# Kernel tuning notes

Measured on AMD Instinct MI355X. Metric: run time of the kernel, lower is better.

The kernel has to match this reference:

```python
import jax, jax.numpy as jnp
import numpy as np

IN_F, OUT_F, R = 4096, 4096, 16
SCALING = 32.0 / R  # lora_alpha / r


def setup_inputs() -> dict:
    key = jax.random.key(0)
    kx, kw, kb, ka, kB = jax.random.split(key, 5)
    bound_w = 1.0 / np.sqrt(IN_F)  # kaiming_uniform a=sqrt(5) on (out,in) -> U(-1/sqrt(in), 1/sqrt(in))
    x = jax.random.normal(kx, (4, 4096, IN_F), dtype=jnp.float32)
    weight = jax.random.uniform(kw, (OUT_F, IN_F), jnp.float32, -bound_w, bound_w)
    bias = jax.random.uniform(kb, (OUT_F,), jnp.float32, -bound_w, bound_w)
    lora_A = jax.random.uniform(ka, (R, IN_F), jnp.float32, -bound_w, bound_w)
    # B is zero-init in the module; use small random values so the LoRA path is exercised
    lora_B = jax.random.normal(kB, (OUT_F, R), dtype=jnp.float32) * 0.01
    return {"x": x, "weight": weight, "bias": bias, "lora_A": lora_A, "lora_B": lora_B}


def reference(x, weight, bias, lora_A, lora_B):
    # base: F.linear(x, W, b) = x @ W.T + b
    base_out = jnp.einsum("bsi,oi->bso", x, weight) + bias
    # low-rank path: (x @ A.T) @ B.T * scaling  (dropout=0 -> identity)
    xr = jnp.einsum("bsi,ri->bsr", x, lora_A)  # [b, s, r]
    lora_out = jnp.einsum("bsr,or->bso", xr, lora_B) * SCALING
    return base_out + lora_out
```

## Files before the change

### kernel.cpp

```cpp
#include <hip/hip_runtime.h>
#include <hip/hip_bf16.h>


typedef __attribute__((ext_vector_type(8))) short bf16x8;
typedef __attribute__((ext_vector_type(4))) float f32x4;
typedef __attribute__((ext_vector_type(4))) unsigned short u16x4;

#define M_DIM 16384
#define N_DIM 4096
#define K_DIM 4096
#define NT 64

__device__ __forceinline__ unsigned short f2bf(float f) {
    unsigned int u = __builtin_bit_cast(unsigned int, f);
    unsigned int r = u + 0x7FFFu + ((u >> 16) & 1u);
    return (unsigned short)(r >> 16);
}

__device__ __forceinline__ void async16(const void* g, void* l) {
    __builtin_amdgcn_global_load_lds(
        (const __attribute__((address_space(1))) unsigned int*)g,
        (__attribute__((address_space(3))) unsigned int*)l,
        16, 0, 0);
}

__global__ void __launch_bounds__(256) cast_x_kernel(
    const float4* __restrict__ x, u16x4* __restrict__ y, int n4) {
    int i = blockIdx.x * blockDim.x + threadIdx.x;
    int stride = gridDim.x * blockDim.x;
    for (; i < n4; i += stride) {
        float4 v = x[i];
        u16x4 o = { f2bf(v.x), f2bf(v.y), f2bf(v.z), f2bf(v.w) };
        y[i] = o;
    }
}

__global__ void __launch_bounds__(256) weff_kernel(
    const float* __restrict__ W, const float* __restrict__ lA,
    const float* __restrict__ lB, unsigned short* __restrict__ out) {
    constexpr int K = K_DIM, R = 16;
    constexpr float S = 2.0f;
    int o = blockIdx.x;
    int t = threadIdx.x;
    float b[R];
#pragma unroll
    for (int r = 0; r < R; ++r) b[r] = lB[o * R + r];
#pragma unroll
    for (int c = 0; c < 4; ++c) {
        int i = c * 1024 + t * 4;
        float4 wv = *reinterpret_cast<const float4*>(&W[o * K + i]);
        float sx = 0.f, sy = 0.f, sz = 0.f, sw = 0.f;
#pragma unroll
        for (int r = 0; r < R; ++r) {
            float4 a = *reinterpret_cast<const float4*>(&lA[r * K + i]);
            sx += b[r] * a.x; sy += b[r] * a.y;
            sz += b[r] * a.z; sw += b[r] * a.w;
        }
        u16x4 ov = { f2bf(wv.x + S * sx), f2bf(wv.y + S * sy),
                     f2bf(wv.z + S * sz), f2bf(wv.w + S * sw) };
        *reinterpret_cast<u16x4*>(&out[o * K + i]) = ov;
    }
}

#define STAGE(G, h, tt, bsel, moff)                                           \
    do {                                                                      \
        const unsigned short* g0 = (G) +                                      \
            (size_t)((h) * 128 + wid * 16 + rc) * K_DIM + (tt) * 64 + cc * 8; \
        char* l0 = lds + (bsel) * 65536 + (moff) + (h) * 16384 + wid * 2048;  \
        async16(g0, l0);                                                      \
        async16(g0 + 8 * K_DIM, l0 + 1024);                                   \
    } while (0)

#define LDA_KS(dst, mh, ks, bsel)                                             \
    _Pragma("unroll") for (int mm = 0; mm < 4; ++mm)                          \
        dst[mm] = *(const bf16x8*)(lds + (bsel) * 65536 +                     \
            ((aBase + ((mh) * 4 + mm) * 2048) ^ ((ks) << 6)));

#define LDB_KS(ks, bsel)                                                      \
    _Pragma("unroll") for (int nn = 0; nn < 4; ++nn)                          \
        br[nn][ks] = *(const bf16x8*)(lds + (bsel) * 65536 +                  \
            ((bBase + nn * 2048) ^ ((ks) << 6)));

#define MMQ_KS(src, mh, ks)                                                   \
    __builtin_amdgcn_s_setprio(1);                                            \
    _Pragma("unroll") for (int mm = 0; mm < 4; ++mm)                          \
    _Pragma("unroll") for (int nn = 0; nn < 4; ++nn)                          \
        acc[(mh) * 4 + mm][nn] = __builtin_amdgcn_mfma_f32_16x16x32_bf16(     \
            src[mm], br[nn][ks], acc[(mh) * 4 + mm][nn], 0, 0, 0);            \
    __builtin_amdgcn_s_setprio(0)

#define CFENCE() asm volatile("" ::: "memory")
#define WAIT_LGKM(n)                                                          \
    asm volatile("s_waitcnt lgkmcnt(" #n ")" ::: "memory");                   \
    __builtin_amdgcn_sched_barrier(0)

#define KTILE(t)                                                              \
    {                                                                         \
        const int bs_ = (t) & 1, bo_ = bs_ ^ 1;                               \
        LDA_KS(arE, 0, 0, bs_);                                   \
        LDB_KS(0, bs_);                                           \
        if ((t) + 1 < NT) STAGE(Ag, 0, (t) + 1, bo_, 0);                      \
        LDA_KS(arO, 1, 0, bs_);                                    \
        WAIT_LGKM(4);                                                         \
        MMQ_KS(arE, 0, 0);                                                    \
        if ((t) + 1 < NT) STAGE(Ag, 1, (t) + 1, bo_, 0);                      \
        LDA_KS(arE, 0, 1, bs_);                \
        LDB_KS(1, bs_);                                           \
        WAIT_LGKM(8);                                                         \
        MMQ_KS(arO, 1, 0);                                                    \
        LDA_KS(arO, 1, 1, bs_);                                    \
        WAIT_LGKM(4);                                                         \
        MMQ_KS(arE, 0, 1);                                                    \
        CFENCE();                                                             \
        __builtin_amdgcn_s_barrier();    \
        CFENCE();                                                             \
        if ((t) + 2 < NT) STAGE(Bg, 0, (t) + 2, bs_, 32768);                  \
        WAIT_LGKM(0);                                                         \
        MMQ_KS(arO, 1, 1);                                                    \
        if ((t) + 2 < NT) STAGE(Bg, 1, (t) + 2, bs_, 32768);                  \
        if ((t) < NT - 2) {                                                   \
            asm volatile("s_waitcnt vmcnt(4)" ::: "memory");                  \
        } else {                                                              \
            asm volatile("s_waitcnt vmcnt(0)" ::: "memory");                  \
        }                                                                     \
        __builtin_amdgcn_s_barrier();                                         \
        CFENCE();                                                             \
    }

__global__ void __launch_bounds__(512, 2) gemmks_kernel(
    const unsigned short* __restrict__ A,
    const unsigned short* __restrict__ B,
    const float* __restrict__ bias,
    float* __restrict__ C) {
    __shared__ __align__(1024) char lds[131072];

    const int tid = threadIdx.x;
    const int lane = tid & 63, wid = tid >> 6;
    const int wm = wid >> 2, wn = wid & 3;
    const int lr = lane & 15, lg = lane >> 4;

    const int bid = blockIdx.x;
    const int swz = (bid & 7) * 128 + (bid >> 3);
    const int bm = swz >> 4, bn = swz & 15;

    const unsigned short* Ag = A + (size_t)bm * 256 * K_DIM;
    const unsigned short* Bg = B + (size_t)bn * 256 * K_DIM;

    const int lam = lane ^ (lane >> 3);
    const int rc = lam >> 3, cc = lam & 7;

    const int kx0 = (lg * 16) ^ ((lr & 7) << 4);
    const int aBase = (wm * 128 + lr) * 128 + kx0;
    const int bBase = 32768 + (wn * 64 + lr) * 128 + kx0;

    f32x4 acc[8][4] = {};
    bf16x8 arE[4], arO[4], br[4][2];

    STAGE(Bg, 0, 0, 0, 32768);
    STAGE(Bg, 1, 0, 0, 32768);
    STAGE(Ag, 0, 0, 0, 0);
    STAGE(Ag, 1, 0, 0, 0);
    STAGE(Bg, 0, 1, 1, 32768);
    STAGE(Bg, 1, 1, 1, 32768);
    asm volatile("s_waitcnt vmcnt(4)" ::: "memory");
    __builtin_amdgcn_s_barrier();
    CFENCE();

#pragma unroll 2
    for (int t = 0; t < NT; ++t) {
        KTILE(t);
    }

    const int row0 = bm * 256 + wm * 128;
    const int col0 = bn * 256 + wn * 64;
#pragma unroll
    for (int n = 0; n < 4; ++n) {
        const int col = col0 + n * 16 + lr;
        const float bv = bias[col];
#pragma unroll
        for (int m = 0; m < 8; ++m) {
            const int r0 = row0 + m * 16 + lg * 4;
#pragma unroll
            for (int r = 0; r < 4; ++r)
                C[(size_t)(r0 + r) * N_DIM + col] = acc[m][n][r] + bv;
        }
    }
}

extern "C" void kernel_launch(void* const* d_in, const int* in_sizes, int n_in,
                              void* d_out, int out_size, void* d_ws, size_t ws_size,
                              hipStream_t stream) {
    const float* x    = (const float*)d_in[0];
    const float* W    = (const float*)d_in[1];
    const float* bias = (const float*)d_in[2];
    const float* lA   = (const float*)d_in[3];
    const float* lB   = (const float*)d_in[4];
    float* out = (float*)d_out;

    unsigned short* xb   = (unsigned short*)d_ws;
    unsigned short* weff = (unsigned short*)((char*)d_ws + 134217728);

    cast_x_kernel<<<2048, 256, 0, stream>>>((const float4*)x, (u16x4*)xb,
                                            M_DIM * K_DIM / 4);
    weff_kernel<<<N_DIM, 256, 0, stream>>>(W, lA, lB, weff);
    gemmks_kernel<<<(M_DIM / 256) * (N_DIM / 256), 512, 0, stream>>>(
        xb, weff, bias, out);
}
```

Measured before the change: 593.2 us.

## Pre-swizzle operands into MFMA fragment layout and switch to 32x32x16 MFMA

The cast and weight-fusion kernels now write bf16 operands directly in a fragment-major layout, so each 32x16 MFMA fragment is a contiguous 1 KB block. The GEMM can then stage with simple linear async copies and read LDS without XOR swizzles. It also moves from 16x16x32 to 32x32x16 MFMA instructions, which need fewer instructions and fewer LDS reads per unit of work. In exchange, the cast kernel's global reads become less coalesced, accumulators now take 16-float vectors, and the epilogue store pattern changes.

```diff
diff --git a/kernel.cpp b/kernel.cpp
--- a/kernel.cpp
+++ b/kernel.cpp
@@ -3,7 +3,7 @@
 
 
 typedef __attribute__((ext_vector_type(8))) short bf16x8;
-typedef __attribute__((ext_vector_type(4))) float f32x4;
+typedef __attribute__((ext_vector_type(16))) float f32x16;
 typedef __attribute__((ext_vector_type(4))) unsigned short u16x4;
 
 #define M_DIM 16384
@@ -25,13 +25,20 @@
 }
 
 __global__ void __launch_bounds__(256) cast_x_kernel(
-    const float4* __restrict__ x, u16x4* __restrict__ y, int n4) {
-    int i = blockIdx.x * blockDim.x + threadIdx.x;
-    int stride = gridDim.x * blockDim.x;
-    for (; i < n4; i += stride) {
-        float4 v = x[i];
-        u16x4 o = { f2bf(v.x), f2bf(v.y), f2bf(v.z), f2bf(v.w) };
-        y[i] = o;
+    const float* __restrict__ x, unsigned short* __restrict__ y) {
+    const int total = 512 * 256 * 64;
+    int idx = blockIdx.x * 256 + threadIdx.x;
+    const int stride = gridDim.x * 256;
+    for (; idx < total; idx += stride) {
+        const int frag = idx >> 6, l = idx & 63;
+        const int m = ((frag >> 8) << 5) + (l & 31);
+        const int k = ((frag & 255) << 4) + ((l >> 5) << 3);
+        const float4* px = reinterpret_cast<const float4*>(&x[(size_t)m * K_DIM + k]);
+        float4 a = px[0], b = px[1];
+        unsigned short r[8] = { f2bf(a.x), f2bf(a.y), f2bf(a.z), f2bf(a.w),
+                                f2bf(b.x), f2bf(b.y), f2bf(b.z), f2bf(b.w) };
+        *reinterpret_cast<bf16x8*>(&y[((size_t)frag << 9) + (l << 3)]) =
+            *reinterpret_cast<const bf16x8*>(r);
     }
 }
 
@@ -58,35 +65,50 @@
         }
         u16x4 ov = { f2bf(wv.x + S * sx), f2bf(wv.y + S * sy),
                      f2bf(wv.z + S * sz), f2bf(wv.w + S * sw) };
-        *reinterpret_cast<u16x4*>(&out[o * K + i]) = ov;
-    }
-}
-
-#define STAGE(G, h, tt, bsel, moff)                                           \
-    do {                                                                      \
-        const unsigned short* g0 = (G) +                                      \
-            (size_t)((h) * 128 + wid * 16 + rc) * K_DIM + (tt) * 64 + cc * 8; \
-        char* l0 = lds + (bsel) * 65536 + (moff) + (h) * 16384 + wid * 2048;  \
-        async16(g0, l0);                                                      \
-        async16(g0 + 8 * K_DIM, l0 + 1024);                                   \
-    } while (0)
-
-#define LDA_KS(dst, mh, ks, bsel)                                             \
-    _Pragma("unroll") for (int mm = 0; mm < 4; ++mm)                          \
-        dst[mm] = *(const bf16x8*)(lds + (bsel) * 65536 +                     \
-            ((aBase + ((mh) * 4 + mm) * 2048) ^ ((ks) << 6)));
-
-#define LDB_KS(ks, bsel)                                                      \
-    _Pragma("unroll") for (int nn = 0; nn < 4; ++nn)                          \
-        br[nn][ks] = *(const bf16x8*)(lds + (bsel) * 65536 +                  \
-            ((bBase + nn * 2048) ^ ((ks) << 6)));
-
-#define MMQ_KS(src, mh, ks)                                                   \
+        const int frag = (o >> 5) * 256 + (i >> 4);
+        const int lane_ = (o & 31) + (((i >> 3) & 1) << 5);
+        *reinterpret_cast<u16x4*>(
+            &out[((size_t)frag << 9) + (lane_ << 3) + (i & 7)]) = ov;
+    }
+}
+
+#define ASTAGE(t, bsel, jlo, jhi)                                             \
+    _Pragma("unroll") for (int j = (jlo); j <= (jhi); ++j) {                  \
+        const int g = wid * 4 + j;                                            \
+        async16(A + (((size_t)(bm * 8 + (g >> 2)) * 256 + (t) * 4 + (g & 3))  \
+                     << 9) + (lane << 3),                                     \
+                lds + (bsel) * 65536 + g * 1024 + (lane << 4));               \
+    }
+
+#define BSTAGE(t, bsel)                                                       \
+    _Pragma("unroll") for (int j = 0; j < 4; ++j) {                           \
+        const int g = wid * 4 + j;                                            \
+        async16(B + (((size_t)(bn * 8 + (g >> 2)) * 256 + (t) * 4 + (g & 3))  \
+                     << 9) + (lane << 3),                                     \
+                lds + (bsel) * 65536 + 32768 + g * 1024 + (lane << 4));       \
+    }
+
+#define LDA32(dst, mh, kh, bsel)                                              \
+    _Pragma("unroll") for (int mm = 0; mm < 2; ++mm)                          \
+    _Pragma("unroll") for (int kk = 0; kk < 2; ++kk)                          \
+        dst[mm * 2 + kk] = *(const bf16x8*)(lds + (bsel) * 65536 +            \
+            (((wm * 4 + (mh) * 2 + mm) * 4 + (kh) * 2 + kk) << 10) +          \
+            (lane << 4));
+
+#define LDB32(dst, kh, bsel)                                                  \
+    _Pragma("unroll") for (int nn = 0; nn < 2; ++nn)                          \
+    _Pragma("unroll") for (int kk = 0; kk < 2; ++kk)                          \
+        dst[nn * 2 + kk] = *(const bf16x8*)(lds + (bsel) * 65536 + 32768 +    \
+            (((wn * 2 + nn) * 4 + (kh) * 2 + kk) << 10) + (lane << 4));
+
+#define MMQ(asrc, bsrc, mh)                                                   \
     __builtin_amdgcn_s_setprio(1);                                            \
-    _Pragma("unroll") for (int mm = 0; mm < 4; ++mm)                          \
-    _Pragma("unroll") for (int nn = 0; nn < 4; ++nn)                          \
-        acc[(mh) * 4 + mm][nn] = __builtin_amdgcn_mfma_f32_16x16x32_bf16(     \
-            src[mm], br[nn][ks], acc[(mh) * 4 + mm][nn], 0, 0, 0);            \
+    _Pragma("unroll") for (int kk = 0; kk < 2; ++kk)                          \
+    _Pragma("unroll") for (int mm = 0; mm < 2; ++mm)                          \
+    _Pragma("unroll") for (int nn = 0; nn < 2; ++nn)                          \
+        acc[(mh) * 2 + mm][nn] = __builtin_amdgcn_mfma_f32_32x32x16_bf16(     \
+            asrc[mm * 2 + kk], bsrc[nn * 2 + kk], acc[(mh) * 2 + mm][nn],     \
+            0, 0, 0);                                                         \
     __builtin_amdgcn_s_setprio(0)
 
 #define CFENCE() asm volatile("" ::: "memory")
@@ -97,27 +119,26 @@
 #define KTILE(t)                                                              \
     {                                                                         \
         const int bs_ = (t) & 1, bo_ = bs_ ^ 1;                               \
-        LDA_KS(arE, 0, 0, bs_);                                   \
-        LDB_KS(0, bs_);                                           \
-        if ((t) + 1 < NT) STAGE(Ag, 0, (t) + 1, bo_, 0);                      \
-        LDA_KS(arO, 1, 0, bs_);                                    \
+        LDA32(arE, 0, 0, bs_);                                    \
+        LDB32(br0, 0, bs_);                                       \
+        if ((t) + 1 < NT) ASTAGE((t) + 1, bo_, 0, 1);                         \
+        LDA32(arO, 1, 0, bs_);                                     \
         WAIT_LGKM(4);                                                         \
-        MMQ_KS(arE, 0, 0);                                                    \
-        if ((t) + 1 < NT) STAGE(Ag, 1, (t) + 1, bo_, 0);                      \
-        LDA_KS(arE, 0, 1, bs_);                \
-        LDB_KS(1, bs_);                                           \
+        MMQ(arE, br0, 0);                                                     \
+        if ((t) + 1 < NT) ASTAGE((t) + 1, bo_, 2, 3);                         \
+        LDA32(arE2, 0, 1, bs_);                                   \
+        LDB32(br1, 1, bs_);                                       \
         WAIT_LGKM(8);                                                         \
-        MMQ_KS(arO, 1, 0);                                                    \
-        LDA_KS(arO, 1, 1, bs_);                                    \
+        MMQ(arO, br0, 1);                                                     \
+        LDA32(arO2, 1, 1, bs_);                                    \
         WAIT_LGKM(4);                                                         \
-        MMQ_KS(arE, 0, 1);                                                    \
+        MMQ(arE2, br1, 0);                                                    \
         CFENCE();                                                             \
-        __builtin_amdgcn_s_barrier();    \
+        __builtin_amdgcn_s_barrier();      \
         CFENCE();                                                             \
-        if ((t) + 2 < NT) STAGE(Bg, 0, (t) + 2, bs_, 32768);                  \
+        if ((t) + 2 < NT) BSTAGE((t) + 2, bs_);                               \
         WAIT_LGKM(0);                                                         \
-        MMQ_KS(arO, 1, 1);                                                    \
-        if ((t) + 2 < NT) STAGE(Bg, 1, (t) + 2, bs_, 32768);                  \
+        MMQ(arO2, br1, 1);                                                    \
         if ((t) < NT - 2) {                                                   \
             asm volatile("s_waitcnt vmcnt(4)" ::: "memory");                  \
         } else {                                                              \
@@ -127,7 +148,7 @@
         CFENCE();                                                             \
     }
 
-__global__ void __launch_bounds__(512, 2) gemmks_kernel(
+__global__ void __launch_bounds__(512, 2) gemmfl_kernel(
     const unsigned short* __restrict__ A,
     const unsigned short* __restrict__ B,
     const float* __restrict__ bias,
@@ -137,31 +158,18 @@
     const int tid = threadIdx.x;
     const int lane = tid & 63, wid = tid >> 6;
     const int wm = wid >> 2, wn = wid & 3;
-    const int lr = lane & 15, lg = lane >> 4;
+    const int lc = lane & 31, hi = lane >> 5;
 
     const int bid = blockIdx.x;
     const int swz = (bid & 7) * 128 + (bid >> 3);
     const int bm = swz >> 4, bn = swz & 15;
 
-    const unsigned short* Ag = A + (size_t)bm * 256 * K_DIM;
-    const unsigned short* Bg = B + (size_t)bn * 256 * K_DIM;
-
-    const int lam = lane ^ (lane >> 3);
-    const int rc = lam >> 3, cc = lam & 7;
-
-    const int kx0 = (lg * 16) ^ ((lr & 7) << 4);
-    const int aBase = (wm * 128 + lr) * 128 + kx0;
-    const int bBase = 32768 + (wn * 64 + lr) * 128 + kx0;
-
-    f32x4 acc[8][4] = {};
-    bf16x8 arE[4], arO[4], br[4][2];
-
-    STAGE(Bg, 0, 0, 0, 32768);
-    STAGE(Bg, 1, 0, 0, 32768);
-    STAGE(Ag, 0, 0, 0, 0);
-    STAGE(Ag, 1, 0, 0, 0);
-    STAGE(Bg, 0, 1, 1, 32768);
-    STAGE(Bg, 1, 1, 1, 32768);
+    f32x16 acc[4][2] = {};
+    bf16x8 arE[4], arO[4], arE2[4], arO2[4], br0[4], br1[4];
+
+    BSTAGE(0, 0);
+    ASTAGE(0, 0, 0, 3);
+    BSTAGE(1, 1);
     asm volatile("s_waitcnt vmcnt(4)" ::: "memory");
     __builtin_amdgcn_s_barrier();
     CFENCE();
@@ -174,15 +182,19 @@
     const int row0 = bm * 256 + wm * 128;
     const int col0 = bn * 256 + wn * 64;
 #pragma unroll
-    for (int n = 0; n < 4; ++n) {
-        const int col = col0 + n * 16 + lr;
+    for (int n = 0; n < 2; ++n) {
+        const int col = col0 + n * 32 + lc;
         const float bv = bias[col];
 #pragma unroll
-        for (int m = 0; m < 8; ++m) {
-            const int r0 = row0 + m * 16 + lg * 4;
-#pragma unroll
-            for (int r = 0; r < 4; ++r)
-                C[(size_t)(r0 + r) * N_DIM + col] = acc[m][n][r] + bv;
+        for (int m = 0; m < 4; ++m) {
+#pragma unroll
+            for (int g = 0; g < 4; ++g) {
+#pragma unroll
+                for (int r = 0; r < 4; ++r) {
+                    const int row = row0 + m * 32 + g * 8 + 4 * hi + r;
+                    C[(size_t)row * N_DIM + col] = acc[m][n][g * 4 + r] + bv;
+                }
+            }
         }
     }
 }
@@ -200,9 +212,8 @@
     unsigned short* xb   = (unsigned short*)d_ws;
     unsigned short* weff = (unsigned short*)((char*)d_ws + 134217728);
 
-    cast_x_kernel<<<2048, 256, 0, stream>>>((const float4*)x, (u16x4*)xb,
-                                            M_DIM * K_DIM / 4);
+    cast_x_kernel<<<4096, 256, 0, stream>>>(x, xb);
     weff_kernel<<<N_DIM, 256, 0, stream>>>(W, lA, lB, weff);
-    gemmks_kernel<<<(M_DIM / 256) * (N_DIM / 256), 512, 0, stream>>>(
+    gemmfl_kernel<<<(M_DIM / 256) * (N_DIM / 256), 512, 0, stream>>>(
         xb, weff, bias, out);
 }
```

Measured after the change: 631.4 us. +6.4%, slower.
